# Kernel optimization log

Hardware: AMD Instinct MI355X
Metric: run time of the kernel (lower is better)

## Reference

```python
import jax, jax.numpy as jnp
import numpy as np

LN_EPS = 1e-5


def _ln(x, g, b):
    mu = jnp.mean(x, -1, keepdims=True)
    xc = x - mu
    inv = jax.lax.rsqrt(jnp.mean(xc * xc, -1, keepdims=True) + LN_EPS)
    return xc * inv * g + b


def _subm_conv(x, nbr, W, b):
    # Submanifold 3D conv via rulebook gather-GEMM-accumulate.
    # x: [N, Cin], nbr: [N, K] neighbor row ids (-1 = missing), W: [K, Cin, Cout], b: [Cout]
    N = x.shape[0]
    xp = jnp.concatenate([x, jnp.zeros((1, x.shape[1]), x.dtype)], 0)  # sentinel zero row
    idx = jnp.where(nbr < 0, N, nbr)  # missing neighbors -> zero row
    acc0 = jnp.zeros((N, W.shape[-1]), x.dtype) + b
    def body(acc, xs):
        i, Wk = xs  # i: [N], Wk: [Cin, Cout]
        return acc + xp[i] @ Wk, None
    acc, _ = jax.lax.scan(body, acc0, (idx.T, W))
    return acc


def _blk1(x, W, b, g, be):  # 1x1x1 SubMConv + LN + ReLU
    return jax.nn.relu(_ln(x @ W + b, g, be))


def _blk3(x, nbr, W, b, g, be):  # 3x3x3 SubMConv + LN + ReLU
    return jax.nn.relu(_ln(_subm_conv(x, nbr, W, b), g, be))


def setup_inputs() -> dict:
    rng = np.random.default_rng(0)
    B, D, Npb, K = 2, 160, 131072, 27
    dim, half = 64, 32
    # Build random sparse voxel set and the rulebook (neighbor table) like spconv does.
    lookup = np.full((B, D, D, D), -1, np.int64)
    coords = np.zeros((B * Npb, 3), np.int64)
    for b in range(B):
        lin = np.sort(rng.choice(D * D * D, size=Npb, replace=False))
        z, y, x = np.unravel_index(lin, (D, D, D))
        rows = np.arange(b * Npb, (b + 1) * Npb)
        lookup[b, z, y, x] = rows
        coords[rows] = np.stack([z, y, x], 1)
    bidx = np.repeat(np.arange(B), Npb)
    offs = np.stack(np.meshgrid(np.arange(-1, 2), np.arange(-1, 2), np.arange(-1, 2), indexing="ij"), -1).reshape(K, 3)
    nz = coords[:, None, :] + offs[None]  # [N, K, 3]
    valid = ((nz >= 0) & (nz < D)).all(-1)
    nzc = np.clip(nz, 0, D - 1)
    nbr = lookup[bidx[:, None], nzc[..., 0], nzc[..., 1], nzc[..., 2]]
    nbr = np.where(valid, nbr, -1).astype(np.int32)

    key = jax.random.key(0)
    ks = iter(jax.random.split(key, 16))
    f32 = jnp.float32
    d = {"voxel_features": jax.random.normal(next(ks), (B * Npb, dim), f32),
         "nbr_idx": jnp.asarray(nbr)}
    def lnp(c):
        return jnp.ones((c,), f32), jnp.zeros((c,), f32)
    d["W1"] = 0.05 * jax.random.normal(next(ks), (dim, dim), f32); d["b1"] = jnp.zeros((dim,), f32); d["g1"], d["be1"] = lnp(dim)
    d["W2"] = 0.05 * jax.random.normal(next(ks), (dim, dim), f32); d["b2"] = jnp.zeros((dim,), f32); d["g2"], d["be2"] = lnp(dim)
    d["W3"] = 0.05 * jax.random.normal(next(ks), (K, dim, half), f32); d["b3"] = jnp.zeros((half,), f32); d["g3"], d["be3"] = lnp(half)
    d["W4"] = 0.05 * jax.random.normal(next(ks), (K, half, half), f32); d["b4"] = jnp.zeros((half,), f32); d["g4"], d["be4"] = lnp(half)
    d["W5"] = 0.05 * jax.random.normal(next(ks), (K, half, half), f32); d["b5"] = jnp.zeros((half,), f32); d["g5"], d["be5"] = lnp(half)
    d["W6"] = 0.05 * jax.random.normal(next(ks), (K, half, half), f32); d["b6"] = jnp.zeros((half,), f32); d["g6"], d["be6"] = lnp(half)
    d["W7"] = 0.05 * jax.random.normal(next(ks), (4 * dim, dim), f32); d["b7"] = jnp.zeros((dim,), f32); d["g7"], d["be7"] = lnp(dim)
    return d


def reference(voxel_features, nbr_idx,
              W1, b1, g1, be1, W2, b2, g2, be2,
              W3, b3, g3, be3, W4, b4, g4, be4,
              W5, b5, g5, be5, W6, b6, g6, be6,
              W7, b7, g7, be7):
    x = voxel_features
    f1 = _blk1(x, W1, b1, g1, be1)
    f2 = _blk1(x, W2, b2, g2, be2)
    feats = [f1, f2]
    f2 = _blk3(f2, nbr_idx, W3, b3, g3, be3); feats.append(f2)
    f2 = _blk3(f2, nbr_idx, W4, b4, g4, be4); feats.append(f2)
    f2 = _blk3(f2, nbr_idx, W5, b5, g5, be5); feats.append(f2)
    f2 = _blk3(f2, nbr_idx, W6, b6, g6, be6); feats.append(f2)
    cat = jnp.concatenate(feats, -1)  # [N, 4*dim]
    return _blk1(cat, W7, b7, g7, be7)
```

## Files before the change

### kernel.cpp

```cpp
#include <hip/hip_runtime.h>

typedef __attribute__((ext_vector_type(4))) float  float4_;
typedef __attribute__((ext_vector_type(8))) short  short8;
typedef __attribute__((ext_vector_type(8))) __bf16 bf16x8;

__device__ inline unsigned short f2bf(float f) {
    unsigned u = __builtin_bit_cast(unsigned, f);
    u += 0x7FFFu + ((u >> 16) & 1u);
    return (unsigned short)(u >> 16);
}

__device__ inline float4_ mfma16(bf16x8 a, bf16x8 b, float4_ c) {
    return __builtin_amdgcn_mfma_f32_16x16x32_bf16(a, b, c, 0, 0, 0);
}

__device__ inline void packW_one(const float* __restrict__ src, unsigned short* __restrict__ dst,
                                 int cin, int cout, int e) {
    int f = e >> 9, i = e & 511, lane = i >> 3, t = i & 7;
    int ntn = cout >> 4, ctn = cin >> 5;
    int nt = f % ntn;
    int rest = f / ntn;
    int ct = rest % ctn;
    int k = rest / ctn;
    int c = ct * 32 + (lane >> 4) * 8 + t;
    int j = nt * 16 + (lane & 15);
    dst[e] = f2bf(src[(k * cin + c) * cout + j]);
}

__global__ void pack_all_kernel(
    const float* __restrict__ W1, const float* __restrict__ W2,
    const float* __restrict__ W3, const float* __restrict__ W4,
    const float* __restrict__ W5, const float* __restrict__ W6,
    const float* __restrict__ W7,
    unsigned short* cat, unsigned short* Wp12, unsigned short* Wp3,
    unsigned short* Wp4, unsigned short* Wp5, unsigned short* Wp6,
    unsigned short* Wp7, int N) {
    int e = blockIdx.x * 256 + threadIdx.x;
    if (e < 8192) {
        int f = e >> 9, i = e & 511, lane = i >> 3, t = i & 7;
        int nt = f & 7, ct = f >> 3;
        int c = ct * 32 + (lane >> 4) * 8 + t;
        int j = nt * 16 + (lane & 15);
        float v = (j < 64) ? W1[c * 64 + j] : W2[c * 64 + (j - 64)];
        Wp12[e] = f2bf(v);
        return;
    }
    e -= 8192;
    if (e < 57344) { if (e < 55296) packW_one(W3, Wp3, 64, 32, e); else Wp3[e] = 0; return; }
    e -= 57344;
    if (e < 28672) { if (e < 27648) packW_one(W4, Wp4, 32, 32, e); else Wp4[e] = 0; return; }
    e -= 28672;
    if (e < 28672) { if (e < 27648) packW_one(W5, Wp5, 32, 32, e); else Wp5[e] = 0; return; }
    e -= 28672;
    if (e < 28672) { if (e < 27648) packW_one(W6, Wp6, 32, 32, e); else Wp6[e] = 0; return; }
    e -= 28672;
    if (e < 16384) { packW_one(W7, Wp7, 256, 64, e); return; }
    e -= 16384;
    if (e < 128) ((unsigned*)(cat + (size_t)N * 256))[e] = 0;
}

__global__ __launch_bounds__(256) void plan_kernel(const int* __restrict__ nbr,
                                                   unsigned int* __restrict__ kmask,
                                                   int* __restrict__ cidx, int N) {
    __shared__ int snb[6912];
    __shared__ unsigned tm[16];
    int tid = threadIdx.x;
    if (tid < 16) tm[tid] = 0u;
    __syncthreads();
    long base = (long)blockIdx.x * 6912;
#pragma unroll
    for (int i = 0; i < 27; i++) {
        int j = i * 256 + tid;
        int v = nbr[base + j];
        snb[j] = v;
        if (v >= 0) {
            unsigned r = (unsigned)j / 27u;
            unsigned k = (unsigned)j - r * 27u;
            atomicOr(&tm[r >> 4], 1u << k);
        }
    }
    __syncthreads();
    int g = tid >> 4, r = tid & 15;
    unsigned m = tm[g];
    int t = blockIdx.x * 16 + g;
    int* cp = cidx + (long)t * 432;
    int j = 0;
#pragma unroll
    for (int k = 0; k < 27; k++) {
        if (m >> k & 1u) {
            int v = snb[(g * 16 + r) * 27 + k];
            cp[j * 16 + r] = (v < 0) ? N : v;
            j++;
        }
    }
    if (r == 0) kmask[t] = m;
}

__global__ __launch_bounds__(256) void blk12_kernel(
    const float* __restrict__ x, unsigned short* cat,
    const unsigned short* __restrict__ Wp,
    const float* __restrict__ b1, const float* __restrict__ g1, const float* __restrict__ be1,
    const float* __restrict__ b2, const float* __restrict__ g2, const float* __restrict__ be2) {
    int tid = threadIdx.x, lane = tid & 63, wv = tid >> 6;
    int l15 = lane & 15, q = lane >> 4;
    long base = ((long)blockIdx.x * 4 + wv) * 16;

    float4_ acc[8];
#pragma unroll
    for (int i = 0; i < 8; i++) acc[i] = (float4_){0.f, 0.f, 0.f, 0.f};

#pragma unroll
    for (int kt = 0; kt < 2; kt++) {
        const float* xp = x + (base + l15) * 64 + kt * 32 + q * 8;
        float4_ f0 = *(const float4_*)xp;
        float4_ f1 = *(const float4_*)(xp + 4);
        short8 as;
        as[0] = (short)f2bf(f0[0]); as[1] = (short)f2bf(f0[1]);
        as[2] = (short)f2bf(f0[2]); as[3] = (short)f2bf(f0[3]);
        as[4] = (short)f2bf(f1[0]); as[5] = (short)f2bf(f1[1]);
        as[6] = (short)f2bf(f1[2]); as[7] = (short)f2bf(f1[3]);
        bf16x8 a = __builtin_bit_cast(bf16x8, as);
        const unsigned short* wp = Wp + (size_t)kt * 8 * 512;
#pragma unroll
        for (int nt = 0; nt < 8; nt++) {
            bf16x8 w = *(const bf16x8*)(wp + nt * 512 + lane * 8);
            acc[nt] = mfma16(a, w, acc[nt]);
        }
    }

    float bc[8], gc[8], bec[8];
#pragma unroll
    for (int nt = 0; nt < 8; nt++) {
        int j = nt * 16 + l15;
        if (j < 64) { bc[nt] = b1[j]; gc[nt] = g1[j]; bec[nt] = be1[j]; }
        else        { bc[nt] = b2[j - 64]; gc[nt] = g2[j - 64]; bec[nt] = be2[j - 64]; }
    }

#pragma unroll
    for (int r = 0; r < 4; r++) {
        long row = base + q * 4 + r;
        float v[8], s0 = 0.f, s1 = 0.f, q0 = 0.f, q1 = 0.f;
#pragma unroll
        for (int nt = 0; nt < 4; nt++) { v[nt] = acc[nt][r] + bc[nt]; s0 += v[nt]; q0 += v[nt] * v[nt]; }
#pragma unroll
        for (int nt = 4; nt < 8; nt++) { v[nt] = acc[nt][r] + bc[nt]; s1 += v[nt]; q1 += v[nt] * v[nt]; }
#pragma unroll
        for (int m = 1; m < 16; m <<= 1) {
            s0 += __shfl_xor(s0, m); q0 += __shfl_xor(q0, m);
            s1 += __shfl_xor(s1, m); q1 += __shfl_xor(q1, m);
        }
        float mu0 = s0 * (1.f / 64), var0 = q0 * (1.f / 64) - mu0 * mu0, inv0 = rsqrtf(var0 + 1e-5f);
        float mu1 = s1 * (1.f / 64), var1 = q1 * (1.f / 64) - mu1 * mu1, inv1 = rsqrtf(var1 + 1e-5f);
        unsigned short* cp = cat + row * 256;
#pragma unroll
        for (int nt = 0; nt < 4; nt++) {
            float y = fmaxf((v[nt] - mu0) * inv0 * gc[nt] + bec[nt], 0.f);
            cp[nt * 16 + l15] = f2bf(y);
        }
#pragma unroll
        for (int nt = 4; nt < 8; nt++) {
            float y = fmaxf((v[nt] - mu1) * inv1 * gc[nt] + bec[nt], 0.f);
            cp[nt * 16 + l15] = f2bf(y);
        }
    }
}

template <int CT, int D>
__global__ __launch_bounds__(256) void conv_kernel(
    unsigned short* cat, const int* __restrict__ cidx,
    const unsigned int* __restrict__ kmask,
    const unsigned short* __restrict__ Wp,
    const float* __restrict__ bb, const float* __restrict__ gg, const float* __restrict__ bee,
    int in_off, int out_off, int N) {
    int tid = threadIdx.x, lane = tid & 63, wv = tid >> 6;
    int l15 = lane & 15, q = lane >> 4;

    int cpx = (int)(gridDim.x >> 3);
    int sb = ((int)blockIdx.x & 7) * cpx + ((int)blockIdx.x >> 3);
    int t = sb * 4 + wv;
    long base = (long)t * 16;

    unsigned m = __builtin_amdgcn_readfirstlane(kmask[t]);

    int ke[27];
    unsigned mm = m;
#pragma unroll
    for (int j = 0; j < 27; j++) {
        ke[j] = mm ? (int)__builtin_ctz(mm) : 27;
        mm &= mm - 1u;
    }

    float4_ acc[2];
    acc[0] = (float4_){0.f, 0.f, 0.f, 0.f};
    acc[1] = (float4_){0.f, 0.f, 0.f, 0.f};

    const unsigned short* catp = cat + in_off + q * 8;
    const unsigned short* wl = Wp + lane * 8;
    const int* cx = cidx + (long)t * 432 + l15;

    bf16x8 f[D + 1][CT];
    bf16x8 wr[3][CT][2];
    int ci[3];

    int ci0[D + 2];
#pragma unroll
    for (int j = 0; j < D + 2; j++) ci0[j] = cx[j * 16];

#pragma unroll
    for (int kk = 0; kk < 2; kk++)
#pragma unroll
        for (int ct = 0; ct < CT; ct++)
#pragma unroll
            for (int nt = 0; nt < 2; nt++)
                wr[kk][ct][nt] =
                    *(const bf16x8*)(wl + ((size_t)((ke[kk] * CT + ct) * 2 + nt)) * 512);

#pragma unroll
    for (int j = 0; j < D; j++) {
        int v = ci0[j];
        size_t s = (size_t)(v < 0 ? 0 : (v > N ? N : v));
#pragma unroll
        for (int ct = 0; ct < CT; ct++)
            f[j][ct] = *(const bf16x8*)(catp + s * 256 + ct * 32);
    }
    ci[D % 3] = ci0[D];
    ci[(D + 1) % 3] = ci0[D + 1];

#pragma unroll
    for (int k = 0; k < 27; k++) {
        if (k + 2 < 27) {
#pragma unroll
            for (int ct = 0; ct < CT; ct++)
#pragma unroll
                for (int nt = 0; nt < 2; nt++)
                    wr[(k + 2) % 3][ct][nt] =
                        *(const bf16x8*)(wl + ((size_t)((ke[k + 2] * CT + ct) * 2 + nt)) * 512);
        }
        if (k + D < 27) {
            int v = ci[(k + D) % 3];
            size_t s = (size_t)(v < 0 ? 0 : (v > N ? N : v));
#pragma unroll
            for (int ct = 0; ct < CT; ct++)
                f[(k + D) % (D + 1)][ct] = *(const bf16x8*)(catp + s * 256 + ct * 32);
        }
        if (k + D + 2 < 27) ci[(k + D + 2) % 3] = cx[(k + D + 2) * 16];
#pragma unroll
        for (int ct = 0; ct < CT; ct++) {
            acc[0] = mfma16(f[k % (D + 1)][ct], wr[k % 3][ct][0], acc[0]);
            acc[1] = mfma16(f[k % (D + 1)][ct], wr[k % 3][ct][1], acc[1]);
        }
    }

    float b0c = bb[l15], b1c = bb[16 + l15];
    float g0c = gg[l15], g1c = gg[16 + l15];
    float be0c = bee[l15], be1c = bee[16 + l15];

#pragma unroll
    for (int r = 0; r < 4; r++) {
        long row = base + q * 4 + r;
        float v0 = acc[0][r] + b0c;
        float v1 = acc[1][r] + b1c;
        float s = v0 + v1, sq = v0 * v0 + v1 * v1;
#pragma unroll
        for (int mh = 1; mh < 16; mh <<= 1) { s += __shfl_xor(s, mh); sq += __shfl_xor(sq, mh); }
        float mu = s * (1.f / 32), var = sq * (1.f / 32) - mu * mu, inv = rsqrtf(var + 1e-5f);
        float y0 = fmaxf((v0 - mu) * inv * g0c + be0c, 0.f);
        float y1 = fmaxf((v1 - mu) * inv * g1c + be1c, 0.f);
        unsigned short* cp = cat + row * 256 + out_off;
        cp[l15] = f2bf(y0);
        cp[16 + l15] = f2bf(y1);
    }
}

__global__ __launch_bounds__(256) void blk7_kernel(
    const unsigned short* __restrict__ cat, const unsigned short* __restrict__ Wp,
    const float* __restrict__ b, const float* __restrict__ g, const float* __restrict__ be,
    float* __restrict__ out) {
    int tid = threadIdx.x, lane = tid & 63, wv = tid >> 6;
    int l15 = lane & 15, q = lane >> 4;
    long base = ((long)blockIdx.x * 4 + wv) * 16;

    float4_ acc[4];
#pragma unroll
    for (int i = 0; i < 4; i++) acc[i] = (float4_){0.f, 0.f, 0.f, 0.f};

#pragma unroll
    for (int kt = 0; kt < 8; kt++) {
        bf16x8 a = *(const bf16x8*)(cat + (base + l15) * 256 + kt * 32 + q * 8);
        const unsigned short* wp = Wp + (size_t)kt * 4 * 512;
#pragma unroll
        for (int nt = 0; nt < 4; nt++) {
            bf16x8 w = *(const bf16x8*)(wp + nt * 512 + lane * 8);
            acc[nt] = mfma16(a, w, acc[nt]);
        }
    }

    float bc[4], gc[4], bec[4];
#pragma unroll
    for (int nt = 0; nt < 4; nt++) {
        int j = nt * 16 + l15;
        bc[nt] = b[j]; gc[nt] = g[j]; bec[nt] = be[j];
    }

#pragma unroll
    for (int r = 0; r < 4; r++) {
        long row = base + q * 4 + r;
        float v[4], s = 0.f, sq = 0.f;
#pragma unroll
        for (int nt = 0; nt < 4; nt++) { v[nt] = acc[nt][r] + bc[nt]; s += v[nt]; sq += v[nt] * v[nt]; }
#pragma unroll
        for (int m = 1; m < 16; m <<= 1) { s += __shfl_xor(s, m); sq += __shfl_xor(sq, m); }
        float mu = s * (1.f / 64), var = sq * (1.f / 64) - mu * mu, inv = rsqrtf(var + 1e-5f);
#pragma unroll
        for (int nt = 0; nt < 4; nt++) {
            float y = fmaxf((v[nt] - mu) * inv * gc[nt] + bec[nt], 0.f);
            out[row * 64 + nt * 16 + l15] = y;
        }
    }
}

extern "C" void kernel_launch(void* const* d_in, const int* in_sizes, int n_in,
                              void* d_out, int out_size, void* d_ws, size_t ws_size,
                              hipStream_t stream) {
    const int N = in_sizes[0] / 64;

    const float* x   = (const float*)d_in[0];
    const int*   nbr = (const int*)d_in[1];
    const float* W1 = (const float*)d_in[2];
    const float* b1 = (const float*)d_in[3];
    const float* g1 = (const float*)d_in[4];
    const float* be1 = (const float*)d_in[5];
    const float* W2 = (const float*)d_in[6];
    const float* b2 = (const float*)d_in[7];
    const float* g2 = (const float*)d_in[8];
    const float* be2 = (const float*)d_in[9];
    const float* W3 = (const float*)d_in[10];
    const float* b3 = (const float*)d_in[11];
    const float* g3 = (const float*)d_in[12];
    const float* be3 = (const float*)d_in[13];
    const float* W4 = (const float*)d_in[14];
    const float* b4 = (const float*)d_in[15];
    const float* g4 = (const float*)d_in[16];
    const float* be4 = (const float*)d_in[17];
    const float* W5 = (const float*)d_in[18];
    const float* b5 = (const float*)d_in[19];
    const float* g5 = (const float*)d_in[20];
    const float* be5 = (const float*)d_in[21];
    const float* W6 = (const float*)d_in[22];
    const float* b6 = (const float*)d_in[23];
    const float* g6 = (const float*)d_in[24];
    const float* be6 = (const float*)d_in[25];
    const float* W7 = (const float*)d_in[26];
    const float* b7 = (const float*)d_in[27];
    const float* g7 = (const float*)d_in[28];
    const float* be7 = (const float*)d_in[29];

    unsigned short* ws   = (unsigned short*)d_ws;
    unsigned short* cat  = ws;
    unsigned short* Wp12 = cat + (size_t)(N + 1) * 256;
    unsigned short* Wp3  = Wp12 + 8192;
    unsigned short* Wp4  = Wp3 + 57344;
    unsigned short* Wp5  = Wp4 + 28672;
    unsigned short* Wp6  = Wp5 + 28672;
    unsigned short* Wp7  = Wp6 + 28672;
    unsigned int*   kmask = (unsigned int*)(Wp7 + 16384);
    int*            cidx  = (int*)(kmask + N / 16);

    pack_all_kernel<<<657, 256, 0, stream>>>(W1, W2, W3, W4, W5, W6, W7,
                                             cat, Wp12, Wp3, Wp4, Wp5, Wp6, Wp7, N);
    plan_kernel<<<N / 256, 256, 0, stream>>>(nbr, kmask, cidx, N);

    blk12_kernel<<<N / 64, 256, 0, stream>>>(x, cat, Wp12, b1, g1, be1, b2, g2, be2);
    conv_kernel<2, 3><<<N / 64, 256, 0, stream>>>(cat, cidx, kmask, Wp3, b3, g3, be3, 64, 128, N);
    conv_kernel<1, 4><<<N / 64, 256, 0, stream>>>(cat, cidx, kmask, Wp4, b4, g4, be4, 128, 160, N);
    conv_kernel<1, 4><<<N / 64, 256, 0, stream>>>(cat, cidx, kmask, Wp5, b5, g5, be5, 160, 192, N);
    conv_kernel<1, 4><<<N / 64, 256, 0, stream>>>(cat, cidx, kmask, Wp6, b6, g6, be6, 192, 224, N);
    blk7_kernel<<<N / 64, 256, 0, stream>>>(cat, Wp7, b7, g7, be7, (float*)d_out);
}
```

Baseline: 524.5 us.

## Skip absent kernel offsets per tile with trip-count specialized conv loops

The conv loop now runs only over the kernel offsets actually present in each 16-row tile. The count is rounded up to a multiple of 4 and dispatched through a switch to template instances of the unrolled core, instead of always iterating all 27 offsets. The plan kernel now also writes a per-tile byte table of active offsets and pads the index table with zero-row entries. It stores neighbor indices pre-scaled to byte offsets, which removes the clamp and multiply from the gather. The costs are larger code size (seven unrolled variants per conv kernel), a bigger workspace, and a little extra plan-kernel work.

```diff
diff --git a/kernel.cpp b/kernel.cpp
--- a/kernel.cpp
+++ b/kernel.cpp
@@ -3,6 +3,7 @@
 typedef __attribute__((ext_vector_type(4))) float  float4_;
 typedef __attribute__((ext_vector_type(8))) short  short8;
 typedef __attribute__((ext_vector_type(8))) __bf16 bf16x8;
+typedef __attribute__((ext_vector_type(4))) unsigned uint4_;
 
 __device__ inline unsigned short f2bf(float f) {
     unsigned u = __builtin_bit_cast(unsigned, f);
@@ -61,7 +62,8 @@
 
 __global__ __launch_bounds__(256) void plan_kernel(const int* __restrict__ nbr,
                                                    unsigned int* __restrict__ kmask,
-                                                   int* __restrict__ cidx, int N) {
+                                                   unsigned int* __restrict__ cidx,
+                                                   unsigned char* __restrict__ ktab, int N) {
     __shared__ int snb[6912];
     __shared__ unsigned tm[16];
     int tid = threadIdx.x;
@@ -83,17 +85,26 @@
     int g = tid >> 4, r = tid & 15;
     unsigned m = tm[g];
     int t = blockIdx.x * 16 + g;
-    int* cp = cidx + (long)t * 432;
+    unsigned* cp = cidx + (long)t * 448;
     int j = 0;
 #pragma unroll
     for (int k = 0; k < 27; k++) {
         if (m >> k & 1u) {
             int v = snb[(g * 16 + r) * 27 + k];
-            cp[j * 16 + r] = (v < 0) ? N : v;
+            cp[j * 16 + r] = (unsigned)(v < 0 ? N : v) * 512u;
             j++;
         }
     }
-    if (r == 0) kmask[t] = m;
+    for (; j < 28; j++) cp[j * 16 + r] = (unsigned)N * 512u;
+    if (r == 0) {
+        kmask[t] = m;
+        unsigned char* kt = ktab + (long)t * 32;
+        int jj = 0;
+#pragma unroll
+        for (int k = 0; k < 27; k++)
+            if (m >> k & 1u) kt[jj++] = (unsigned char)k;
+        for (; jj < 32; jj++) kt[jj] = 27;
+    }
 }
 
 __global__ __launch_bounds__(256) void blk12_kernel(
@@ -165,9 +176,69 @@
     }
 }
 
+template <int CT, int D, int NS>
+__device__ __forceinline__ void conv_core(
+    float4_ acc[2], const char* catb, const unsigned* cx,
+    const unsigned* kt8, const unsigned short* wl) {
+    bf16x8 f[D + 1][CT];
+    bf16x8 wr[3][CT][2];
+    unsigned cv[3];
+
+#define KB(k) ((kt8[(k) >> 2] >> (((k) & 3) * 8)) & 0xFFu)
+
+    unsigned cv0[D + 2];
+#pragma unroll
+    for (int j = 0; j < D + 2; j++) cv0[j] = cx[j * 16];
+
+#pragma unroll
+    for (int kk = 0; kk < 2; kk++) {
+        unsigned wo = KB(kk) * (CT * 1024u);
+#pragma unroll
+        for (int ct = 0; ct < CT; ct++)
+#pragma unroll
+            for (int nt = 0; nt < 2; nt++)
+                wr[kk][ct][nt] = *(const bf16x8*)(wl + wo + (ct * 2 + nt) * 512);
+    }
+
+#pragma unroll
+    for (int j = 0; j < D; j++) {
+#pragma unroll
+        for (int ct = 0; ct < CT; ct++)
+            f[j][ct] = *(const bf16x8*)(catb + (size_t)cv0[j] + ct * 64);
+    }
+    cv[D % 3] = cv0[D];
+    cv[(D + 1) % 3] = cv0[D + 1];
+
+#pragma unroll
+    for (int k = 0; k < NS; k++) {
+        if (k + 2 < NS) {
+            unsigned wo = KB(k + 2) * (CT * 1024u);
+#pragma unroll
+            for (int ct = 0; ct < CT; ct++)
+#pragma unroll
+                for (int nt = 0; nt < 2; nt++)
+                    wr[(k + 2) % 3][ct][nt] = *(const bf16x8*)(wl + wo + (ct * 2 + nt) * 512);
+        }
+        if (k + D < NS) {
+            unsigned voff = cv[(k + D) % 3];
+#pragma unroll
+            for (int ct = 0; ct < CT; ct++)
+                f[(k + D) % (D + 1)][ct] = *(const bf16x8*)(catb + (size_t)voff + ct * 64);
+        }
+        if (k + D + 2 < NS) cv[(k + D + 2) % 3] = cx[(k + D + 2) * 16];
+#pragma unroll
+        for (int ct = 0; ct < CT; ct++) {
+            acc[0] = mfma16(f[k % (D + 1)][ct], wr[k % 3][ct][0], acc[0]);
+            acc[1] = mfma16(f[k % (D + 1)][ct], wr[k % 3][ct][1], acc[1]);
+        }
+    }
+#undef KB
+}
+
 template <int CT, int D>
 __global__ __launch_bounds__(256) void conv_kernel(
-    unsigned short* cat, const int* __restrict__ cidx,
+    unsigned short* cat, const unsigned int* __restrict__ cidx,
+    const unsigned char* __restrict__ ktab,
     const unsigned int* __restrict__ kmask,
     const unsigned short* __restrict__ Wp,
     const float* __restrict__ bb, const float* __restrict__ gg, const float* __restrict__ bee,
@@ -181,74 +252,28 @@
     long base = (long)t * 16;
 
     unsigned m = __builtin_amdgcn_readfirstlane(kmask[t]);
-
-    int ke[27];
-    unsigned mm = m;
-#pragma unroll
-    for (int j = 0; j < 27; j++) {
-        ke[j] = mm ? (int)__builtin_ctz(mm) : 27;
-        mm &= mm - 1u;
-    }
+    int trips = (__popc(m) + 3) >> 2;
+
+    const char* catb = (const char*)cat + (size_t)in_off * 2 + q * 16;
+    const unsigned* cx = cidx + (long)t * 448 + l15;
+    const unsigned short* wl = Wp + lane * 8;
+
+    uint4_ kv0 = *(const uint4_*)(ktab + (long)t * 32);
+    uint4_ kv1 = *(const uint4_*)(ktab + (long)t * 32 + 16);
+    unsigned kt8[8] = {kv0[0], kv0[1], kv0[2], kv0[3], kv1[0], kv1[1], kv1[2], kv1[3]};
 
     float4_ acc[2];
     acc[0] = (float4_){0.f, 0.f, 0.f, 0.f};
     acc[1] = (float4_){0.f, 0.f, 0.f, 0.f};
 
-    const unsigned short* catp = cat + in_off + q * 8;
-    const unsigned short* wl = Wp + lane * 8;
-    const int* cx = cidx + (long)t * 432 + l15;
-
-    bf16x8 f[D + 1][CT];
-    bf16x8 wr[3][CT][2];
-    int ci[3];
-
-    int ci0[D + 2];
-#pragma unroll
-    for (int j = 0; j < D + 2; j++) ci0[j] = cx[j * 16];
-
-#pragma unroll
-    for (int kk = 0; kk < 2; kk++)
-#pragma unroll
-        for (int ct = 0; ct < CT; ct++)
-#pragma unroll
-            for (int nt = 0; nt < 2; nt++)
-                wr[kk][ct][nt] =
-                    *(const bf16x8*)(wl + ((size_t)((ke[kk] * CT + ct) * 2 + nt)) * 512);
-
-#pragma unroll
-    for (int j = 0; j < D; j++) {
-        int v = ci0[j];
-        size_t s = (size_t)(v < 0 ? 0 : (v > N ? N : v));
-#pragma unroll
-        for (int ct = 0; ct < CT; ct++)
-            f[j][ct] = *(const bf16x8*)(catp + s * 256 + ct * 32);
-    }
-    ci[D % 3] = ci0[D];
-    ci[(D + 1) % 3] = ci0[D + 1];
-
-#pragma unroll
-    for (int k = 0; k < 27; k++) {
-        if (k + 2 < 27) {
-#pragma unroll
-            for (int ct = 0; ct < CT; ct++)
-#pragma unroll
-                for (int nt = 0; nt < 2; nt++)
-                    wr[(k + 2) % 3][ct][nt] =
-                        *(const bf16x8*)(wl + ((size_t)((ke[k + 2] * CT + ct) * 2 + nt)) * 512);
-        }
-        if (k + D < 27) {
-            int v = ci[(k + D) % 3];
-            size_t s = (size_t)(v < 0 ? 0 : (v > N ? N : v));
-#pragma unroll
-            for (int ct = 0; ct < CT; ct++)
-                f[(k + D) % (D + 1)][ct] = *(const bf16x8*)(catp + s * 256 + ct * 32);
-        }
-        if (k + D + 2 < 27) ci[(k + D + 2) % 3] = cx[(k + D + 2) * 16];
-#pragma unroll
-        for (int ct = 0; ct < CT; ct++) {
-            acc[0] = mfma16(f[k % (D + 1)][ct], wr[k % 3][ct][0], acc[0]);
-            acc[1] = mfma16(f[k % (D + 1)][ct], wr[k % 3][ct][1], acc[1]);
-        }
+    switch (trips) {
+        case 1: conv_core<CT, D, 4>(acc, catb, cx, kt8, wl); break;
+        case 2: conv_core<CT, D, 8>(acc, catb, cx, kt8, wl); break;
+        case 3: conv_core<CT, D, 12>(acc, catb, cx, kt8, wl); break;
+        case 4: conv_core<CT, D, 16>(acc, catb, cx, kt8, wl); break;
+        case 5: conv_core<CT, D, 20>(acc, catb, cx, kt8, wl); break;
+        case 6: conv_core<CT, D, 24>(acc, catb, cx, kt8, wl); break;
+        default: conv_core<CT, D, 28>(acc, catb, cx, kt8, wl); break;
     }
 
     float b0c = bb[l15], b1c = bb[16 + l15];
@@ -364,16 +389,17 @@
     unsigned short* Wp6  = Wp5 + 28672;
     unsigned short* Wp7  = Wp6 + 28672;
     unsigned int*   kmask = (unsigned int*)(Wp7 + 16384);
-    int*            cidx  = (int*)(kmask + N / 16);
+    unsigned int*   cidx  = kmask + N / 16;
+    unsigned char*  ktab  = (unsigned char*)(cidx + (size_t)(N / 16) * 448);
 
     pack_all_kernel<<<657, 256, 0, stream>>>(W1, W2, W3, W4, W5, W6, W7,
                                              cat, Wp12, Wp3, Wp4, Wp5, Wp6, Wp7, N);
-    plan_kernel<<<N / 256, 256, 0, stream>>>(nbr, kmask, cidx, N);
+    plan_kernel<<<N / 256, 256, 0, stream>>>(nbr, kmask, cidx, ktab, N);
 
     blk12_kernel<<<N / 64, 256, 0, stream>>>(x, cat, Wp12, b1, g1, be1, b2, g2, be2);
-    conv_kernel<2, 3><<<N / 64, 256, 0, stream>>>(cat, cidx, kmask, Wp3, b3, g3, be3, 64, 128, N);
-    conv_kernel<1, 4><<<N / 64, 256, 0, stream>>>(cat, cidx, kmask, Wp4, b4, g4, be4, 128, 160, N);
-    conv_kernel<1, 4><<<N / 64, 256, 0, stream>>>(cat, cidx, kmask, Wp5, b5, g5, be5, 160, 192, N);
-    conv_kernel<1, 4><<<N / 64, 256, 0, stream>>>(cat, cidx, kmask, Wp6, b6, g6, be6, 192, 224, N);
+    conv_kernel<2, 3><<<N / 64, 256, 0, stream>>>(cat, cidx, ktab, kmask, Wp3, b3, g3, be3, 64, 128, N);
+    conv_kernel<1, 4><<<N / 64, 256, 0, stream>>>(cat, cidx, ktab, kmask, Wp4, b4, g4, be4, 128, 160, N);
+    conv_kernel<1, 4><<<N / 64, 256, 0, stream>>>(cat, cidx, ktab, kmask, Wp5, b5, g5, be5, 160, 192, N);
+    conv_kernel<1, 4><<<N / 64, 256, 0, stream>>>(cat, cidx, ktab, kmask, Wp6, b6, g6, be6, 192, 224, N);
     blk7_kernel<<<N / 64, 256, 0, stream>>>(cat, Wp7, b7, g7, be7, (float*)d_out);
 }
```

Result: faster. 434.6 us (-17.2%).
